# Optimization experiments

Hardware: AMD Instinct MI355X
Metric: run time of the kernel (lower is better)

## Reference

```python
import jax, jax.numpy as jnp
import numpy as np

B, S, D = 4, 2048, 512
H = 8
DEPTH = D // H  # 64


def setup_inputs() -> dict:
    key = jax.random.key(0)
    ks = jax.random.split(key, 6)
    scale = 1.0 / np.sqrt(D)
    return {
        "x": jax.random.normal(ks[0], (B, S, D), dtype=jnp.float32),
        "y": jax.random.normal(ks[1], (B, S, D), dtype=jnp.float32),
        "W_q": jax.random.normal(ks[2], (D, D), dtype=jnp.float32) * scale,
        "W_k": jax.random.normal(ks[3], (D, D), dtype=jnp.float32) * scale,
        "W_v": jax.random.normal(ks[4], (D, D), dtype=jnp.float32) * scale,
        "W_o": jax.random.normal(ks[5], (D, D), dtype=jnp.float32) * scale,
    }


def _split_heads(t):
    # [B, S, D] -> [B, H, S, DEPTH]
    b, s, _ = t.shape
    return t.reshape(b, s, H, DEPTH).transpose(0, 2, 1, 3)


def reference(x, y, W_q, W_k, W_v, W_o):
    q = _split_heads(x @ W_q) * (DEPTH ** -0.5)   # [B,H,Sq,d]
    k = _split_heads(y @ W_k)                      # [B,H,Sk,d]
    v = _split_heads(y @ W_v)                      # [B,H,Sk,d]
    logits = jnp.einsum("bhqd,bhkd->bhqk", q, k)   # [B,H,Sq,Sk]
    weights = jax.nn.softmax(logits, axis=-1)
    attn = jnp.einsum("bhqk,bhkd->bhqd", weights, v)  # [B,H,Sq,d]
    attn = attn.transpose(0, 2, 1, 3).reshape(x.shape[0], x.shape[1], D)
    return attn @ W_o
```

## Files before the change

kernel.cpp:

```cpp
#include <hip/hip_runtime.h>
#include <hip/hip_bf16.h>
#include <math.h>
#include <stdint.h>

#define NB 4
#define NS 2048
#define ND 512
#define NH 8
#define DEP 64

typedef __attribute__((ext_vector_type(8))) short bf16x8;
typedef __attribute__((ext_vector_type(4))) short bf16x4;
typedef __attribute__((ext_vector_type(4))) float f32x4;

#define QSCALE 0.18033688011112042f

__device__ __forceinline__ short f2b(float f) {
  unsigned u = __float_as_uint(f);
  u += 0x7FFF + ((u >> 16) & 1);
  return (short)(u >> 16);
}
__device__ __forceinline__ unsigned pk2(float a, float b) {
  union { __hip_bfloat162 h; unsigned u; } c;
  c.h = __float22bfloat162_rn(float2{a, b});
  return c.u;
}
__device__ __forceinline__ void dma16(const void* g, void* l) {
  __builtin_amdgcn_global_load_lds(
      (const __attribute__((address_space(1))) void*)g,
      (__attribute__((address_space(3))) void*)l, 16, 0, 0);
}

__global__ __launch_bounds__(256) void cast_xy(const float* __restrict__ x,
                                               const float* __restrict__ y,
                                               short* __restrict__ xb,
                                               short* __restrict__ yb) {
  const float* src = blockIdx.y ? y : x;
  short* dst = blockIdx.y ? yb : xb;
  size_t i = ((size_t)blockIdx.x * 256 + threadIdx.x) * 4;
  float4 v = *(const float4*)(src + i);
  bf16x4 o;
  o[0] = f2b(v.x); o[1] = f2b(v.y); o[2] = f2b(v.z); o[3] = f2b(v.w);
  *(bf16x4*)(dst + i) = o;
}

__global__ __launch_bounds__(256) void trans_w(
    const float* __restrict__ W0, const float* __restrict__ W1,
    const float* __restrict__ W2, const float* __restrict__ W3,
    short* __restrict__ T0, short* __restrict__ T1, short* __restrict__ T2,
    short* __restrict__ T3) {
  const float* W = blockIdx.z == 0 ? W0 : blockIdx.z == 1 ? W1
                   : blockIdx.z == 2 ? W2 : W3;
  short* T = blockIdx.z == 0 ? T0 : blockIdx.z == 1 ? T1
             : blockIdx.z == 2 ? T2 : T3;
  __shared__ float tile[64][65];
  const int t = threadIdx.x;
  const int k0 = blockIdx.x * 64, n0 = blockIdx.y * 64;
#pragma unroll
  for (int i = 0; i < 4; ++i) {
    int r = (t >> 4) + i * 16;
    int c = (t & 15) * 4;
    float4 v = *(const float4*)&W[(size_t)(k0 + r) * ND + n0 + c];
    tile[r][c] = v.x; tile[r][c + 1] = v.y;
    tile[r][c + 2] = v.z; tile[r][c + 3] = v.w;
  }
  __syncthreads();
#pragma unroll
  for (int i = 0; i < 4; ++i) {
    int n = (t >> 4) + i * 16;
    int kc = (t & 15) * 4;
    bf16x4 o;
#pragma unroll
    for (int j = 0; j < 4; ++j) o[j] = f2b(tile[kc + j][n]);
    *(bf16x4*)&T[(size_t)(n0 + n) * ND + k0 + kc] = o;
  }
}

__device__ __forceinline__ void gemm_core(const short* __restrict__ A,
                                          const short* __restrict__ Bt,
                                          void* __restrict__ Cout, int mode,
                                          float alpha) {
  __shared__ short As[128 * 64];
  __shared__ short Bs[128 * 64];
  const int t = threadIdx.x;
  const int wave = t >> 6, lane = t & 63;
  const int m = lane & 15, quad = lane >> 4;
  const int m0 = blockIdx.y * 128, n0 = blockIdx.x * 128;
  const int mh = (wave >> 1) * 64, nh = (wave & 1) * 64;
  const int r8 = lane >> 3;
  const int c8 = (lane & 7) ^ r8;
  const int mx7 = m & 7;
  f32x4 acc[4][4];
#pragma unroll
  for (int i = 0; i < 4; ++i)
#pragma unroll
    for (int j = 0; j < 4; ++j) acc[i][j] = (f32x4){0.f, 0.f, 0.f, 0.f};

  for (int k0 = 0; k0 < ND; k0 += 64) {
    __syncthreads();
#pragma unroll
    for (int i = 0; i < 4; ++i) {
      int row = i * 32 + wave * 8 + r8;
      dma16(A + (size_t)(m0 + row) * ND + k0 + c8 * 8,
            As + (i * 256 + wave * 64) * 8);
      dma16(Bt + (size_t)(n0 + row) * ND + k0 + c8 * 8,
            Bs + (i * 256 + wave * 64) * 8);
    }
    __syncthreads();
    bf16x8 af[4][2], bf[4][2];
#pragma unroll
    for (int mt = 0; mt < 4; ++mt)
#pragma unroll
      for (int kc = 0; kc < 2; ++kc)
        af[mt][kc] = *(const bf16x8*)(As + (mh + mt * 16 + m) * 64 +
                                      ((kc * 4 + quad) ^ mx7) * 8);
#pragma unroll
    for (int nt = 0; nt < 4; ++nt)
#pragma unroll
      for (int kc = 0; kc < 2; ++kc)
        bf[nt][kc] = *(const bf16x8*)(Bs + (nh + nt * 16 + m) * 64 +
                                      ((kc * 4 + quad) ^ mx7) * 8);
#pragma unroll
    for (int mt = 0; mt < 4; ++mt)
#pragma unroll
      for (int nt = 0; nt < 4; ++nt)
#pragma unroll
        for (int kc = 0; kc < 2; ++kc)
          acc[mt][nt] = __builtin_amdgcn_mfma_f32_16x16x32_bf16(
              af[mt][kc], bf[nt][kc], acc[mt][nt], 0, 0, 0);
  }
  if (mode == 2) {
#pragma unroll
    for (int mt = 0; mt < 4; ++mt)
#pragma unroll
      for (int nt = 0; nt < 4; ++nt) {
        int row0 = m0 + mh + mt * 16 + quad * 4;
        int col = n0 + nh + nt * 16 + m;
        int b_ = row0 >> 11, s_ = row0 & (NS - 1);
        int h_ = col >> 6, d_ = col & (DEP - 1);
        uint2 p;
        p.x = pk2(acc[mt][nt][0] * alpha, acc[mt][nt][1] * alpha);
        p.y = pk2(acc[mt][nt][2] * alpha, acc[mt][nt][3] * alpha);
        *(uint2*)((short*)Cout +
                  (size_t)((b_ * NH + h_) * DEP + d_) * NS + s_) = p;
      }
  } else {
#pragma unroll
    for (int mt = 0; mt < 4; ++mt)
#pragma unroll
      for (int nt = 0; nt < 4; ++nt)
#pragma unroll
        for (int r = 0; r < 4; ++r) {
          int row = m0 + mh + mt * 16 + quad * 4 + r;
          int col = n0 + nh + nt * 16 + m;
          float v = acc[mt][nt][r] * alpha;
          if (mode == 1)
            ((short*)Cout)[(size_t)row * ND + col] = f2b(v);
          else
            ((float*)Cout)[(size_t)row * ND + col] = v;
        }
  }
}

__global__ __launch_bounds__(256) void qkv_gemm(
    const short* __restrict__ xb, const short* __restrict__ yb,
    const short* __restrict__ Wqt, const short* __restrict__ Wkt,
    const short* __restrict__ Wvt, short* __restrict__ Qb,
    short* __restrict__ Kb, short* __restrict__ Vtb) {
  if (blockIdx.z == 0)
    gemm_core(xb, Wqt, Qb, 1, QSCALE);
  else if (blockIdx.z == 1)
    gemm_core(yb, Wkt, Kb, 1, 1.0f);
  else
    gemm_core(yb, Wvt, Vtb, 2, 1.0f);
}

__global__ __launch_bounds__(256) void out_gemm(const short* __restrict__ Ab,
                                                const short* __restrict__ Wot,
                                                float* __restrict__ out) {
  gemm_core(Ab, Wot, out, 0, 1.0f);
}

__global__ __launch_bounds__(256) void attn_mfma(const short* __restrict__ Qb,
                                                 const short* __restrict__ Kb,
                                                 const short* __restrict__ Vtb,
                                                 short* __restrict__ Ob) {
  __shared__ short Ks[64 * 64];
  __shared__ short Vts[64 * 64];
  __shared__ short Pt[128 * 64];
  const int t = threadIdx.x;
  const int wave = t >> 6, lane = t & 63;
  const int m = lane & 15, quad = lane >> 4;
  const int bh = blockIdx.y, b = bh >> 3, h = bh & 7;
  const int q0 = blockIdx.x * 128;
  const int wq = wave * 32;
  const size_t rowb = (size_t)b * NS;
  const short* Vtbase = Vtb + (size_t)(bh * DEP) * NS;
  const int r8 = lane >> 3;
  const int c8 = (lane & 7) ^ r8;
  const int mx7 = m & 7;

  bf16x8 qf[2][2];
#pragma unroll
  for (int nt = 0; nt < 2; ++nt)
#pragma unroll
    for (int kc = 0; kc < 2; ++kc)
      qf[nt][kc] = *(const bf16x8*)(Qb + (rowb + q0 + wq + nt * 16 + m) * ND +
                                    h * DEP + kc * 32 + quad * 8);

  float l_[2] = {0.0f, 0.0f};
  f32x4 Ot[4][2];
#pragma unroll
  for (int mt = 0; mt < 4; ++mt)
#pragma unroll
    for (int nt = 0; nt < 2; ++nt) Ot[mt][nt] = (f32x4){0.f, 0.f, 0.f, 0.f};

  for (int kv0 = 0; kv0 < NS; kv0 += 64) {
    __syncthreads();
#pragma unroll
    for (int i = 0; i < 2; ++i) {
      int row = i * 32 + wave * 8 + r8;
      dma16(Kb + (rowb + kv0 + row) * ND + h * DEP + c8 * 8,
            Ks + (i * 256 + wave * 64) * 8);
      dma16(Vtbase + (size_t)row * NS + kv0 + c8 * 8,
            Vts + (i * 256 + wave * 64) * 8);
    }
    __syncthreads();

    f32x4 St[4][2];
#pragma unroll
    for (int mt = 0; mt < 4; ++mt)
#pragma unroll
      for (int nt = 0; nt < 2; ++nt) St[mt][nt] = (f32x4){0.f, 0.f, 0.f, 0.f};
#pragma unroll
    for (int mt = 0; mt < 4; ++mt)
#pragma unroll
      for (int kc = 0; kc < 2; ++kc) {
        bf16x8 kf = *(const bf16x8*)(Ks + (mt * 16 + m) * 64 +
                                     ((kc * 4 + quad) ^ mx7) * 8);
#pragma unroll
        for (int nt = 0; nt < 2; ++nt)
          St[mt][nt] = __builtin_amdgcn_mfma_f32_16x16x32_bf16(
              kf, qf[nt][kc], St[mt][nt], 0, 0, 0);
      }

#pragma unroll
    for (int nt = 0; nt < 2; ++nt) {
      float rs = 0.0f;
#pragma unroll
      for (int mt = 0; mt < 4; ++mt) {
        float p0 = exp2f(St[mt][nt][0]);
        float p1 = exp2f(St[mt][nt][1]);
        float p2 = exp2f(St[mt][nt][2]);
        float p3 = exp2f(St[mt][nt][3]);
        rs += (p0 + p1) + (p2 + p3);
        uint2 pk;
        pk.x = pk2(p0, p1);
        pk.y = pk2(p2, p3);
        *(uint2*)(Pt + (wq + nt * 16 + m) * 64 +
                  ((mt * 2 + (quad >> 1)) ^ mx7) * 8 + (quad & 1) * 4) = pk;
      }
      l_[nt] += rs;
    }

#pragma unroll
    for (int kc = 0; kc < 2; ++kc) {
      bf16x8 pf[2];
#pragma unroll
      for (int nt = 0; nt < 2; ++nt)
        pf[nt] = *(const bf16x8*)(Pt + (wq + nt * 16 + m) * 64 +
                                  ((kc * 4 + quad) ^ mx7) * 8);
#pragma unroll
      for (int mt = 0; mt < 4; ++mt) {
        bf16x8 vf = *(const bf16x8*)(Vts + (mt * 16 + m) * 64 +
                                     ((kc * 4 + quad) ^ mx7) * 8);
#pragma unroll
        for (int nt = 0; nt < 2; ++nt)
          Ot[mt][nt] = __builtin_amdgcn_mfma_f32_16x16x32_bf16(
              vf, pf[nt], Ot[mt][nt], 0, 0, 0);
      }
    }
  }

#pragma unroll
  for (int nt = 0; nt < 2; ++nt) {
    l_[nt] += __shfl_xor(l_[nt], 16, 64);
    l_[nt] += __shfl_xor(l_[nt], 32, 64);
    float linv = 1.0f / l_[nt];
    size_t row = rowb + q0 + wq + nt * 16 + m;
#pragma unroll
    for (int mt = 0; mt < 4; ++mt)
#pragma unroll
      for (int r = 0; r < 4; ++r)
        Ob[row * ND + h * DEP + mt * 16 + quad * 4 + r] =
            f2b(Ot[mt][nt][r] * linv);
  }
}

extern "C" void kernel_launch(void* const* d_in, const int* in_sizes, int n_in,
                              void* d_out, int out_size, void* d_ws,
                              size_t ws_size, hipStream_t stream) {
  const float* x = (const float*)d_in[0];
  const float* y = (const float*)d_in[1];
  const float* Wq = (const float*)d_in[2];
  const float* Wk = (const float*)d_in[3];
  const float* Wv = (const float*)d_in[4];
  const float* Wo = (const float*)d_in[5];
  float* out = (float*)d_out;

  const size_t mat = (size_t)NB * NS * ND;
  const size_t wsz = (size_t)ND * ND;
  short* xb = (short*)d_ws;
  short* yb = xb + mat;
  short* Wqt = yb + mat;
  short* Wkt = Wqt + wsz;
  short* Wvt = Wkt + wsz;
  short* Wot = Wvt + wsz;
  short* Qb = Wot + wsz;
  short* Kb = Qb + mat;
  short* Vtb = Kb + mat;
  short* attnb = xb;

  cast_xy<<<dim3(mat / 1024, 2), 256, 0, stream>>>(x, y, xb, yb);
  trans_w<<<dim3(8, 8, 4), 256, 0, stream>>>(Wq, Wk, Wv, Wo, Wqt, Wkt, Wvt,
                                             Wot);
  qkv_gemm<<<dim3(ND / 128, (NB * NS) / 128, 3), 256, 0, stream>>>(
      xb, yb, Wqt, Wkt, Wvt, Qb, Kb, Vtb);
  attn_mfma<<<dim3(NS / 128, NB * NH), 256, 0, stream>>>(Qb, Kb, Vtb, attnb);
  out_gemm<<<dim3(ND / 128, (NB * NS) / 128), 256, 0, stream>>>(attnb, Wot,
                                                                out);
}
```

Measured before the change: 202.1 us.

## Double-buffer LDS tiles in GEMM and attention, and shrink GEMM N-tile

The GEMM core and the attention kernel now keep two LDS buffers. The next K/V (or A/B) tile is prefetched while the current one is being consumed, so each iteration needs one barrier instead of two. The GEMM block tile also shrinks from 128x128 to 128x64, which doubles the number of blocks in the QKV and output projections for better CU occupancy, at the cost of more redundant A-tile loads. The change relies on the top-of-loop barrier making the asynchronous global-to-LDS copies visible, and it uses more LDS in the attention kernel.

```diff
diff --git a/kernel.cpp b/kernel.cpp
--- a/kernel.cpp
+++ b/kernel.cpp
@@ -80,50 +80,62 @@
                                           const short* __restrict__ Bt,
                                           void* __restrict__ Cout, int mode,
                                           float alpha) {
-  __shared__ short As[128 * 64];
-  __shared__ short Bs[128 * 64];
+  __shared__ short As[2][128 * 64];
+  __shared__ short Bs[2][64 * 64];
   const int t = threadIdx.x;
   const int wave = t >> 6, lane = t & 63;
   const int m = lane & 15, quad = lane >> 4;
-  const int m0 = blockIdx.y * 128, n0 = blockIdx.x * 128;
-  const int mh = (wave >> 1) * 64, nh = (wave & 1) * 64;
+  const int m0 = blockIdx.y * 128, n0 = blockIdx.x * 64;
+  const int mh = (wave >> 1) * 64, nh = (wave & 1) * 32;
   const int r8 = lane >> 3;
   const int c8 = (lane & 7) ^ r8;
   const int mx7 = m & 7;
-  f32x4 acc[4][4];
+  f32x4 acc[4][2];
 #pragma unroll
   for (int i = 0; i < 4; ++i)
 #pragma unroll
-    for (int j = 0; j < 4; ++j) acc[i][j] = (f32x4){0.f, 0.f, 0.f, 0.f};
-
-  for (int k0 = 0; k0 < ND; k0 += 64) {
+    for (int j = 0; j < 2; ++j) acc[i][j] = (f32x4){0.f, 0.f, 0.f, 0.f};
+
+#pragma unroll
+  for (int i = 0; i < 4; ++i)
+    dma16(A + (size_t)(m0 + i * 32 + wave * 8 + r8) * ND + c8 * 8,
+          As[0] + (i * 256 + wave * 64) * 8);
+#pragma unroll
+  for (int i = 0; i < 2; ++i)
+    dma16(Bt + (size_t)(n0 + i * 32 + wave * 8 + r8) * ND + c8 * 8,
+          Bs[0] + (i * 256 + wave * 64) * 8);
+
+  int buf = 0;
+  for (int k0 = 0; k0 < ND; k0 += 64, buf ^= 1) {
     __syncthreads();
-#pragma unroll
-    for (int i = 0; i < 4; ++i) {
-      int row = i * 32 + wave * 8 + r8;
-      dma16(A + (size_t)(m0 + row) * ND + k0 + c8 * 8,
-            As + (i * 256 + wave * 64) * 8);
-      dma16(Bt + (size_t)(n0 + row) * ND + k0 + c8 * 8,
-            Bs + (i * 256 + wave * 64) * 8);
+    if (k0 + 64 < ND) {
+#pragma unroll
+      for (int i = 0; i < 4; ++i)
+        dma16(A + (size_t)(m0 + i * 32 + wave * 8 + r8) * ND + k0 + 64 + c8 * 8,
+              As[buf ^ 1] + (i * 256 + wave * 64) * 8);
+#pragma unroll
+      for (int i = 0; i < 2; ++i)
+        dma16(Bt + (size_t)(n0 + i * 32 + wave * 8 + r8) * ND + k0 + 64 +
+                  c8 * 8,
+              Bs[buf ^ 1] + (i * 256 + wave * 64) * 8);
     }
-    __syncthreads();
-    bf16x8 af[4][2], bf[4][2];
+    bf16x8 af[4][2], bf[2][2];
 #pragma unroll
     for (int mt = 0; mt < 4; ++mt)
 #pragma unroll
       for (int kc = 0; kc < 2; ++kc)
-        af[mt][kc] = *(const bf16x8*)(As + (mh + mt * 16 + m) * 64 +
+        af[mt][kc] = *(const bf16x8*)(As[buf] + (mh + mt * 16 + m) * 64 +
                                       ((kc * 4 + quad) ^ mx7) * 8);
 #pragma unroll
-    for (int nt = 0; nt < 4; ++nt)
+    for (int nt = 0; nt < 2; ++nt)
 #pragma unroll
       for (int kc = 0; kc < 2; ++kc)
-        bf[nt][kc] = *(const bf16x8*)(Bs + (nh + nt * 16 + m) * 64 +
+        bf[nt][kc] = *(const bf16x8*)(Bs[buf] + (nh + nt * 16 + m) * 64 +
                                       ((kc * 4 + quad) ^ mx7) * 8);
 #pragma unroll
     for (int mt = 0; mt < 4; ++mt)
 #pragma unroll
-      for (int nt = 0; nt < 4; ++nt)
+      for (int nt = 0; nt < 2; ++nt)
 #pragma unroll
         for (int kc = 0; kc < 2; ++kc)
           acc[mt][nt] = __builtin_amdgcn_mfma_f32_16x16x32_bf16(
@@ -133,7 +145,7 @@
 #pragma unroll
     for (int mt = 0; mt < 4; ++mt)
 #pragma unroll
-      for (int nt = 0; nt < 4; ++nt) {
+      for (int nt = 0; nt < 2; ++nt) {
         int row0 = m0 + mh + mt * 16 + quad * 4;
         int col = n0 + nh + nt * 16 + m;
         int b_ = row0 >> 11, s_ = row0 & (NS - 1);
@@ -148,7 +160,7 @@
 #pragma unroll
     for (int mt = 0; mt < 4; ++mt)
 #pragma unroll
-      for (int nt = 0; nt < 4; ++nt)
+      for (int nt = 0; nt < 2; ++nt)
 #pragma unroll
         for (int r = 0; r < 4; ++r) {
           int row = m0 + mh + mt * 16 + quad * 4 + r;
@@ -185,8 +197,8 @@
                                                  const short* __restrict__ Kb,
                                                  const short* __restrict__ Vtb,
                                                  short* __restrict__ Ob) {
-  __shared__ short Ks[64 * 64];
-  __shared__ short Vts[64 * 64];
+  __shared__ short Ks[2][64 * 64];
+  __shared__ short Vts[2][64 * 64];
   __shared__ short Pt[128 * 64];
   const int t = threadIdx.x;
   const int wave = t >> 6, lane = t & 63;
@@ -215,17 +227,28 @@
 #pragma unroll
     for (int nt = 0; nt < 2; ++nt) Ot[mt][nt] = (f32x4){0.f, 0.f, 0.f, 0.f};
 
-  for (int kv0 = 0; kv0 < NS; kv0 += 64) {
+#pragma unroll
+  for (int i = 0; i < 2; ++i) {
+    int row = i * 32 + wave * 8 + r8;
+    dma16(Kb + (rowb + row) * ND + h * DEP + c8 * 8,
+          Ks[0] + (i * 256 + wave * 64) * 8);
+    dma16(Vtbase + (size_t)row * NS + c8 * 8,
+          Vts[0] + (i * 256 + wave * 64) * 8);
+  }
+
+  int buf = 0;
+  for (int kv0 = 0; kv0 < NS; kv0 += 64, buf ^= 1) {
     __syncthreads();
-#pragma unroll
-    for (int i = 0; i < 2; ++i) {
-      int row = i * 32 + wave * 8 + r8;
-      dma16(Kb + (rowb + kv0 + row) * ND + h * DEP + c8 * 8,
-            Ks + (i * 256 + wave * 64) * 8);
-      dma16(Vtbase + (size_t)row * NS + kv0 + c8 * 8,
-            Vts + (i * 256 + wave * 64) * 8);
+    if (kv0 + 64 < NS) {
+#pragma unroll
+      for (int i = 0; i < 2; ++i) {
+        int row = i * 32 + wave * 8 + r8;
+        dma16(Kb + (rowb + kv0 + 64 + row) * ND + h * DEP + c8 * 8,
+              Ks[buf ^ 1] + (i * 256 + wave * 64) * 8);
+        dma16(Vtbase + (size_t)row * NS + kv0 + 64 + c8 * 8,
+              Vts[buf ^ 1] + (i * 256 + wave * 64) * 8);
+      }
     }
-    __syncthreads();
 
     f32x4 St[4][2];
 #pragma unroll
@@ -236,7 +259,7 @@
     for (int mt = 0; mt < 4; ++mt)
 #pragma unroll
       for (int kc = 0; kc < 2; ++kc) {
-        bf16x8 kf = *(const bf16x8*)(Ks + (mt * 16 + m) * 64 +
+        bf16x8 kf = *(const bf16x8*)(Ks[buf] + (mt * 16 + m) * 64 +
                                      ((kc * 4 + quad) ^ mx7) * 8);
 #pragma unroll
         for (int nt = 0; nt < 2; ++nt)
@@ -272,7 +295,7 @@
                                   ((kc * 4 + quad) ^ mx7) * 8);
 #pragma unroll
       for (int mt = 0; mt < 4; ++mt) {
-        bf16x8 vf = *(const bf16x8*)(Vts + (mt * 16 + m) * 64 +
+        bf16x8 vf = *(const bf16x8*)(Vts[buf] + (mt * 16 + m) * 64 +
                                      ((kc * 4 + quad) ^ mx7) * 8);
 #pragma unroll
         for (int nt = 0; nt < 2; ++nt)
@@ -324,9 +347,9 @@
   cast_xy<<<dim3(mat / 1024, 2), 256, 0, stream>>>(x, y, xb, yb);
   trans_w<<<dim3(8, 8, 4), 256, 0, stream>>>(Wq, Wk, Wv, Wo, Wqt, Wkt, Wvt,
                                              Wot);
-  qkv_gemm<<<dim3(ND / 128, (NB * NS) / 128, 3), 256, 0, stream>>>(
+  qkv_gemm<<<dim3(ND / 64, (NB * NS) / 128, 3), 256, 0, stream>>>(
       xb, yb, Wqt, Wkt, Wvt, Qb, Kb, Vtb);
   attn_mfma<<<dim3(NS / 128, NB * NH), 256, 0, stream>>>(Qb, Kb, Vtb, attnb);
-  out_gemm<<<dim3(ND / 128, (NB * NS) / 128), 256, 0, stream>>>(attnb, Wot,
-                                                                out);
-}
+  out_gemm<<<dim3(ND / 64, (NB * NS) / 128), 256, 0, stream>>>(attnb, Wot,
+                                                               out);
+}
```

Measured after the change: 205.0 us. Within noise of the previous version (+1.4%).
